# Kernel tuning notes

Hardware: AMD Instinct MI355X
Metric: run time of the kernel (lower is better)

## Reference

```python
import jax, jax.numpy as jnp
import numpy as np

H = 1024      # hidden_size
NH = 16       # num attention heads
NKV = 4       # num kv heads (GQA)
HD = 64       # head_dim
NE = 8        # num experts
TOPK = 2      # experts per token
F = 2048      # expert intermediate size
T = 2048      # num tokens
EPS = 1e-5
THETA = 10000.0


def rmsnorm(x, w):
    var = jnp.mean(x * x, axis=-1, keepdims=True)
    return x * jax.lax.rsqrt(var + EPS) * w


def apply_rope(x, positions):
    # x: [T, nheads, HD], neox style (rotate halves)
    half = HD // 2
    inv_freq = 1.0 / (THETA ** (jnp.arange(half, dtype=jnp.float32) / half))
    ang = positions.astype(jnp.float32)[:, None] * inv_freq  # [T, half]
    cos = jnp.cos(ang)[:, None, :]
    sin = jnp.sin(ang)[:, None, :]
    x1, x2 = x[..., :half], x[..., half:]
    return jnp.concatenate([x1 * cos - x2 * sin, x2 * cos + x1 * sin], axis=-1)


def attention(x, positions, w_qkv, w_o):
    qkv = x @ w_qkv.T                                  # [T, (NH+2*NKV)*HD]
    q = qkv[:, : NH * HD].reshape(T, NH, HD)
    k = qkv[:, NH * HD : (NH + NKV) * HD].reshape(T, NKV, HD)
    v = qkv[:, (NH + NKV) * HD :].reshape(T, NKV, HD)
    q = apply_rope(q, positions)
    k = apply_rope(k, positions)
    rep = NH // NKV
    k = jnp.repeat(k, rep, axis=1)                     # [T, NH, HD]
    v = jnp.repeat(v, rep, axis=1)
    scores = jnp.einsum('qhd,khd->hqk', q, k) * (HD ** -0.5)
    mask = jnp.tril(jnp.ones((T, T), dtype=bool))
    scores = jnp.where(mask[None], scores, jnp.finfo(scores.dtype).min)
    p = jax.nn.softmax(scores, axis=-1)
    o = jnp.einsum('hqk,khd->qhd', p, v).reshape(T, NH * HD)
    return o @ w_o.T


def moe(x, gate_w, w1, w2, w3):
    logits = x @ gate_w.T                              # [T, NE]
    probs = jax.nn.softmax(logits, axis=-1)
    tv, ti = jax.lax.top_k(probs, TOPK)
    tv = tv / jnp.sum(tv, axis=-1, keepdims=True)      # renormalize=True
    dense = jnp.zeros((x.shape[0], NE), x.dtype).at[
        jnp.arange(x.shape[0])[:, None], ti].set(tv)   # [T, NE] sparse routing weights
    h1 = jnp.einsum('th,efh->tef', x, w1)
    h3 = jnp.einsum('th,efh->tef', x, w3)
    act = jax.nn.silu(h1) * h3                         # SwiGLU
    y = jnp.einsum('tef,ehf->teh', act, w2)
    return jnp.einsum('te,teh->th', dense, y)


def setup_inputs() -> dict:
    key = jax.random.key(0)
    ks = jax.random.split(key, 8)
    s = 0.02
    return {
        'positions': jnp.arange(T, dtype=jnp.int32),
        'hidden_states': jax.random.normal(ks[0], (T, H), jnp.float32),
        'w_qkv': jax.random.normal(ks[1], ((NH + 2 * NKV) * HD, H), jnp.float32) * s,
        'w_o': jax.random.normal(ks[2], (H, NH * HD), jnp.float32) * s,
        'norm_in': jnp.ones((H,), jnp.float32),
        'norm_post': jnp.ones((H,), jnp.float32),
        'norm_next': jnp.ones((H,), jnp.float32),
        'gate_w': jax.random.normal(ks[3], (NE, H), jnp.float32) * s,
        'w1': jax.random.normal(ks[4], (NE, F, H), jnp.float32) * s,
        'w2': jax.random.normal(ks[5], (NE, H, F), jnp.float32) * s,
        'w3': jax.random.normal(ks[6], (NE, F, H), jnp.float32) * s,
    }


def reference(positions, hidden_states, w_qkv, w_o, norm_in, norm_post, norm_next,
              gate_w, w1, w2, w3):
    # attn block: pre-norm, attention, residual add
    x = hidden_states + attention(rmsnorm(hidden_states, norm_in), positions, w_qkv, w_o)
    # moe block: pre-norm, sparse MoE, residual add
    x = x + moe(rmsnorm(x, norm_post), gate_w, w1, w2, w3)
    # fused allreduce+norm boundary -> next layer's input norm (world_size=1)
    out = rmsnorm(x, norm_next)
    return (out, x)
```

## Files before the change

### kernel.cpp

```cpp
#include <hip/hip_runtime.h>
#include <hip/hip_bf16.h>
#include <stdint.h>

#define T 2048
#define H 1024
#define NH 16
#define NKV 4
#define HD 64
#define NE 8
#define FF 2048
#define QKVD 1536

typedef unsigned short u16;
typedef short bf16x8 __attribute__((ext_vector_type(8)));
typedef float f32x4 __attribute__((ext_vector_type(4)));

__device__ __forceinline__ float bf2f(u16 u) { return __uint_as_float(((unsigned)u) << 16); }
__device__ __forceinline__ u16 f2b(float f) {
    unsigned u = __float_as_uint(f);
    unsigned r = (u + 0x7FFFu + ((u >> 16) & 1u)) >> 16;
    return (u16)r;
}

#define MFMA(a, b, c) __builtin_amdgcn_mfma_f32_16x16x32_bf16(a, b, c, 0, 0, 0)

__device__ __forceinline__ void gll16(const u16* g, u16* l) {
    __builtin_amdgcn_global_load_lds(
        (const __attribute__((address_space(1))) void*)g,
        (__attribute__((address_space(3))) void*)l, 16, 0, 0);
}

__global__ __launch_bounds__(256) void k_cvt(const float* __restrict__ src,
                                             u16* __restrict__ dst) {
    size_t i = ((size_t)blockIdx.x * 256 + threadIdx.x) * 8;
    float4 a = *(const float4*)(src + i);
    float4 b = *(const float4*)(src + i + 4);
    bf16x8 o;
    o[0] = (short)f2b(a.x); o[1] = (short)f2b(a.y);
    o[2] = (short)f2b(a.z); o[3] = (short)f2b(a.w);
    o[4] = (short)f2b(b.x); o[5] = (short)f2b(b.y);
    o[6] = (short)f2b(b.z); o[7] = (short)f2b(b.w);
    *(bf16x8*)(dst + i) = o;
}

__global__ __launch_bounds__(256) void k_rmsnorm(const float* __restrict__ x,
                                                 const float* __restrict__ w,
                                                 u16* __restrict__ out) {
    int t = blockIdx.x;
    const float* xr = x + (size_t)t * H;
    int base = threadIdx.x * 4;
    float v[4]; float ss = 0.f;
#pragma unroll
    for (int i = 0; i < 4; i++) { v[i] = xr[base + i]; ss += v[i] * v[i]; }
#pragma unroll
    for (int off = 32; off; off >>= 1) ss += __shfl_xor(ss, off, 64);
    __shared__ float red[4];
    int wv = threadIdx.x >> 6, lane = threadIdx.x & 63;
    if (lane == 0) red[wv] = ss;
    __syncthreads();
    float tot = red[0] + red[1] + red[2] + red[3];
    float s = rsqrtf(tot * (1.0f / H) + 1e-5f);
    u16* orow = out + (size_t)t * H;
#pragma unroll
    for (int i = 0; i < 4; i++) orow[base + i] = f2b(v[i] * s * w[base + i]);
}

__global__ __launch_bounds__(256) void k_gemm_qkv(const u16* __restrict__ A,
                                                  const u16* __restrict__ B,
                                                  float* __restrict__ C) {
    __shared__ u16 As[128 * 32], Bs[128 * 32];
    const int K = H;
    int lane = threadIdx.x & 63, wv = threadIdx.x >> 6;
    int l15 = lane & 15, quad = lane >> 4;
    int gm = blockIdx.y * 128, gn = blockIdx.x * 128;
    int c0 = wv * 128 + lane, c1 = c0 + 64;
    int r0 = c0 >> 2, cc0 = (c0 & 3) * 8;
    int r1 = c1 >> 2, cc1 = (c1 & 3) * 8;
    const u16* ag0 = A + (size_t)(gm + r0) * K + cc0;
    const u16* ag1 = A + (size_t)(gm + r1) * K + cc1;
    const u16* bg0 = B + (size_t)(gn + r0) * K + cc0;
    const u16* bg1 = B + (size_t)(gn + r1) * K + cc1;
    u16* la0 = As + (size_t)(wv * 128) * 8;
    u16* la1 = As + (size_t)(wv * 128 + 64) * 8;
    u16* lb0 = Bs + (size_t)(wv * 128) * 8;
    u16* lb1 = Bs + (size_t)(wv * 128 + 64) * 8;
    int am = (wv >> 1) * 64, bn = (wv & 1) * 64;
    f32x4 acc[4][4];
#pragma unroll
    for (int i = 0; i < 4; i++)
#pragma unroll
        for (int j = 0; j < 4; j++) acc[i][j] = (f32x4){0.f, 0.f, 0.f, 0.f};
    for (int kk = 0; kk < K; kk += 32) {
        gll16(ag0 + kk, la0);
        gll16(ag1 + kk, la1);
        gll16(bg0 + kk, lb0);
        gll16(bg1 + kk, lb1);
        __syncthreads();
        bf16x8 a[4], b[4];
#pragma unroll
        for (int i = 0; i < 4; i++) a[i] = *(const bf16x8*)(As + (am + i * 16 + l15) * 32 + quad * 8);
#pragma unroll
        for (int j = 0; j < 4; j++) b[j] = *(const bf16x8*)(Bs + (bn + j * 16 + l15) * 32 + quad * 8);
#pragma unroll
        for (int i = 0; i < 4; i++)
#pragma unroll
            for (int j = 0; j < 4; j++) acc[i][j] = MFMA(a[i], b[j], acc[i][j]);
        __syncthreads();
    }
#pragma unroll
    for (int i = 0; i < 4; i++) {
        int row = gm + am + i * 16 + quad * 4;
#pragma unroll
        for (int j = 0; j < 4; j++) {
            int col = gn + bn + j * 16 + l15;
#pragma unroll
            for (int r = 0; r < 4; r++) C[(size_t)(row + r) * QKVD + col] = acc[i][j][r];
        }
    }
}

__global__ __launch_bounds__(256) void k_rope(const int* __restrict__ positions,
                                              const float* __restrict__ qkv,
                                              u16* __restrict__ qb, u16* __restrict__ kb,
                                              u16* __restrict__ vt) {
    int t = blockIdx.x;
    float p = (float)positions[t];
    const float* base = qkv + (size_t)t * QKVD;
    const float kfreq = -9.210340371976184f / 32.0f;
    for (int idx = threadIdx.x; idx < 512; idx += 256) {
        int hh = idx >> 5, d = idx & 31;
        float ang = p * __expf((float)d * kfreq);
        float cs = cosf(ang), sn = sinf(ang);
        float x1 = base[hh * 64 + d], x2 = base[hh * 64 + d + 32];
        qb[(size_t)t * 1024 + hh * 64 + d] = f2b(x1 * cs - x2 * sn);
        qb[(size_t)t * 1024 + hh * 64 + d + 32] = f2b(x2 * cs + x1 * sn);
    }
    if (threadIdx.x < 128) {
        int idx = threadIdx.x, kh = idx >> 5, d = idx & 31;
        float ang = p * __expf((float)d * kfreq);
        float cs = cosf(ang), sn = sinf(ang);
        const float* kin = base + 1024;
        float x1 = kin[kh * 64 + d], x2 = kin[kh * 64 + d + 32];
        kb[((size_t)t * NKV + kh) * 64 + d] = f2b(x1 * cs - x2 * sn);
        kb[((size_t)t * NKV + kh) * 64 + d + 32] = f2b(x2 * cs + x1 * sn);
    }
    {
        int idx = threadIdx.x;
        vt[(size_t)idx * T + t] = f2b(base[1280 + idx]);
    }
}

__global__ __launch_bounds__(256) void k_attn(const u16* __restrict__ qb,
                                              const u16* __restrict__ kb,
                                              const u16* __restrict__ vt,
                                              u16* __restrict__ o) {
    int h = blockIdx.y;
    int q0 = blockIdx.x * 64;
    int kh = h >> 2;
    int wv = threadIdx.x >> 6, lane = threadIdx.x & 63;
    int l15 = lane & 15, quad = lane >> 4;
    int qw = q0 + wv * 16;
    __shared__ __align__(16) u16 pl[4][16 * 32];

    const u16* qrow = qb + (size_t)(qw + l15) * 1024 + h * 64 + quad * 8;
    bf16x8 aq0 = *(const bf16x8*)qrow;
    bf16x8 aq1 = *(const bf16x8*)(qrow + 32);

    f32x4 oacc[4];
#pragma unroll
    for (int c = 0; c < 4; c++) oacc[c] = (f32x4){0.f, 0.f, 0.f, 0.f};
    float mi[4], li[4];
#pragma unroll
    for (int r = 0; r < 4; r++) { mi[r] = -3e38f; li[r] = 0.f; }

    int ntiles = (q0 >> 5) + 2;
    for (int ti = 0; ti < ntiles; ++ti) {
        int kv0 = ti * 32;
        const u16* kr = kb + (size_t)((kv0 + l15) * NKV + kh) * 64 + quad * 8;
        f32x4 sA = (f32x4){0.f, 0.f, 0.f, 0.f}, sB = (f32x4){0.f, 0.f, 0.f, 0.f};
        sA = MFMA(aq0, *(const bf16x8*)kr, sA);
        sA = MFMA(aq1, *(const bf16x8*)(kr + 32), sA);
        const u16* kr2 = kr + 16 * NKV * 64;
        sB = MFMA(aq0, *(const bf16x8*)kr2, sB);
        sB = MFMA(aq1, *(const bf16x8*)(kr2 + 32), sB);
        int cA = kv0 + l15, cB = cA + 16;
#pragma unroll
        for (int r = 0; r < 4; r++) {
            int qi = qw + quad * 4 + r;
            float a = (cA <= qi) ? sA[r] * 0.125f : -3e38f;
            float b = (cB <= qi) ? sB[r] * 0.125f : -3e38f;
            float mx = fmaxf(a, b);
#pragma unroll
            for (int off = 1; off < 16; off <<= 1) mx = fmaxf(mx, __shfl_xor(mx, off, 64));
            float mn = fmaxf(mi[r], mx);
            float alpha = __expf(mi[r] - mn);
            float pa = __expf(a - mn), pb = __expf(b - mn);
            float ps = pa + pb;
#pragma unroll
            for (int off = 1; off < 16; off <<= 1) ps += __shfl_xor(ps, off, 64);
            li[r] = li[r] * alpha + ps;
            mi[r] = mn;
#pragma unroll
            for (int c = 0; c < 4; c++) oacc[c][r] = oacc[c][r] * alpha;
            int prow = quad * 4 + r;
            pl[wv][prow * 32 + l15] = f2b(pa);
            pl[wv][prow * 32 + 16 + l15] = f2b(pb);
        }
        __syncthreads();
        bf16x8 pfrag = *(const bf16x8*)&pl[wv][l15 * 32 + quad * 8];
#pragma unroll
        for (int c = 0; c < 4; c++) {
            const u16* vr = vt + (size_t)(kh * 64 + c * 16 + l15) * T + kv0 + quad * 8;
            oacc[c] = MFMA(pfrag, *(const bf16x8*)vr, oacc[c]);
        }
        __syncthreads();
    }
#pragma unroll
    for (int r = 0; r < 4; r++) {
        float inv = 1.0f / li[r];
        int row = qw + quad * 4 + r;
#pragma unroll
        for (int c = 0; c < 4; c++)
            o[(size_t)row * 1024 + h * 64 + c * 16 + l15] = f2b(oacc[c][r] * inv);
    }
}

__global__ __launch_bounds__(256) void k_gemm_wo(const u16* __restrict__ A,
                                                 const u16* __restrict__ B,
                                                 const float* __restrict__ hid,
                                                 float* __restrict__ x1) {
    __shared__ u16 As[128 * 32], Bs[128 * 32];
    const int K = H;
    int lane = threadIdx.x & 63, wv = threadIdx.x >> 6;
    int l15 = lane & 15, quad = lane >> 4;
    int gm = blockIdx.y * 128, gn = blockIdx.x * 128;
    int c0 = wv * 128 + lane, c1 = c0 + 64;
    int r0 = c0 >> 2, cc0 = (c0 & 3) * 8;
    int r1 = c1 >> 2, cc1 = (c1 & 3) * 8;
    const u16* ag0 = A + (size_t)(gm + r0) * K + cc0;
    const u16* ag1 = A + (size_t)(gm + r1) * K + cc1;
    const u16* bg0 = B + (size_t)(gn + r0) * K + cc0;
    const u16* bg1 = B + (size_t)(gn + r1) * K + cc1;
    u16* la0 = As + (size_t)(wv * 128) * 8;
    u16* la1 = As + (size_t)(wv * 128 + 64) * 8;
    u16* lb0 = Bs + (size_t)(wv * 128) * 8;
    u16* lb1 = Bs + (size_t)(wv * 128 + 64) * 8;
    int am = (wv >> 1) * 64, bn = (wv & 1) * 64;
    f32x4 acc[4][4];
#pragma unroll
    for (int i = 0; i < 4; i++)
#pragma unroll
        for (int j = 0; j < 4; j++) acc[i][j] = (f32x4){0.f, 0.f, 0.f, 0.f};
    for (int kk = 0; kk < K; kk += 32) {
        gll16(ag0 + kk, la0);
        gll16(ag1 + kk, la1);
        gll16(bg0 + kk, lb0);
        gll16(bg1 + kk, lb1);
        __syncthreads();
        bf16x8 a[4], b[4];
#pragma unroll
        for (int i = 0; i < 4; i++) a[i] = *(const bf16x8*)(As + (am + i * 16 + l15) * 32 + quad * 8);
#pragma unroll
        for (int j = 0; j < 4; j++) b[j] = *(const bf16x8*)(Bs + (bn + j * 16 + l15) * 32 + quad * 8);
#pragma unroll
        for (int i = 0; i < 4; i++)
#pragma unroll
            for (int j = 0; j < 4; j++) acc[i][j] = MFMA(a[i], b[j], acc[i][j]);
        __syncthreads();
    }
#pragma unroll
    for (int i = 0; i < 4; i++) {
        int row = gm + am + i * 16 + quad * 4;
#pragma unroll
        for (int j = 0; j < 4; j++) {
            int col = gn + bn + j * 16 + l15;
#pragma unroll
            for (int r = 0; r < 4; r++) {
                size_t idx = (size_t)(row + r) * H + col;
                x1[idx] = hid[idx] + acc[i][j][r];
            }
        }
    }
}

__global__ void k_zero(int* cnt) { if (threadIdx.x < NE) cnt[threadIdx.x] = 0; }

__global__ __launch_bounds__(256) void k_route(const float* __restrict__ x1,
                                               const float* __restrict__ wpost,
                                               const float* __restrict__ gw,
                                               int* cnt, int* ids, int* rank,
                                               float* gwt) {
    int wv = threadIdx.x >> 6, lane = threadIdx.x & 63;
    int t = blockIdx.x * 4 + wv;
    const float* xr = x1 + (size_t)t * H + lane * 16;
    float pv[16];
    float ss = 0.f;
#pragma unroll
    for (int i = 0; i < 16; i++) { float v = xr[i]; pv[i] = v; ss += v * v; }
#pragma unroll
    for (int off = 32; off; off >>= 1) ss += __shfl_xor(ss, off, 64);
    float s = rsqrtf(ss * (1.0f / H) + 1e-5f);
#pragma unroll
    for (int i = 0; i < 16; i++) pv[i] *= wpost[lane * 16 + i];
    float lg[NE];
#pragma unroll
    for (int e = 0; e < NE; e++) {
        const float* gr = gw + (size_t)e * H + lane * 16;
        float d = 0.f;
#pragma unroll
        for (int i = 0; i < 16; i++) d += pv[i] * gr[i];
#pragma unroll
        for (int off = 32; off; off >>= 1) d += __shfl_xor(d, off, 64);
        lg[e] = d * s;
    }
    if (lane == 0) {
        int i0 = 0; float b0 = lg[0];
        for (int e = 1; e < NE; e++) if (lg[e] > b0) { b0 = lg[e]; i0 = e; }
        int i1 = (i0 == 0) ? 1 : 0; float b1 = lg[i1];
        for (int e = 0; e < NE; e++)
            if (e != i0 && lg[e] > b1) { b1 = lg[e]; i1 = e; }
        float g0 = 1.0f / (1.0f + __expf(b1 - b0));
        float g1 = 1.0f - g0;
        int r0 = atomicAdd(&cnt[i0], 1);
        int r1 = atomicAdd(&cnt[i1], 1);
        ids[2 * t] = i0; ids[2 * t + 1] = i1;
        rank[2 * t] = r0; rank[2 * t + 1] = r1;
        gwt[2 * t] = g0; gwt[2 * t + 1] = g1;
    }
}

__global__ void k_prefix(const int* cnt, int* offs) {
    if (threadIdx.x == 0) {
        int a = 0;
        for (int e = 0; e < NE; e++) { offs[e] = a; a += cnt[e]; }
    }
}

__global__ __launch_bounds__(256) void k_scatter(const int* __restrict__ ids,
                                                 const int* __restrict__ rank,
                                                 const int* __restrict__ offs,
                                                 int* __restrict__ list,
                                                 int* __restrict__ slotof) {
    int t = blockIdx.x * 256 + threadIdx.x;
#pragma unroll
    for (int j = 0; j < 2; j++) {
        int e = ids[2 * t + j];
        int s = offs[e] + rank[2 * t + j];
        list[s] = t;
        slotof[2 * t + j] = s;
    }
}

__global__ __launch_bounds__(256, 2) void k_gemm1(const u16* __restrict__ xnp,
                                                  const u16* __restrict__ w1,
                                                  const u16* __restrict__ w3,
                                                  const int* __restrict__ cnt,
                                                  const int* __restrict__ offs,
                                                  const int* __restrict__ list,
                                                  u16* __restrict__ act) {
    int e = blockIdx.z;
    int ce = cnt[e], oe = offs[e];
    int gm = blockIdx.y * 128;
    if (gm >= ce) return;
    __shared__ u16 As[128 * 32], B1s[128 * 32], B3s[128 * 32];
    const int K = H;
    int lane = threadIdx.x & 63, wv = threadIdx.x >> 6;
    int l15 = lane & 15, quad = lane >> 4;
    int gn = blockIdx.x * 128;
    int c0 = wv * 128 + lane, c1 = c0 + 64;
    int r0 = c0 >> 2, cc0 = (c0 & 3) * 8;
    int r1 = c1 >> 2, cc1 = (c1 & 3) * 8;
    int tok0 = list[min(oe + gm + r0, oe + ce - 1)];
    int tok1 = list[min(oe + gm + r1, oe + ce - 1)];
    const u16* ag0 = xnp + (size_t)tok0 * K + cc0;
    const u16* ag1 = xnp + (size_t)tok1 * K + cc1;
    const u16* B1 = w1 + (size_t)e * FF * H;
    const u16* B3 = w3 + (size_t)e * FF * H;
    const u16* b1g0 = B1 + (size_t)(gn + r0) * K + cc0;
    const u16* b1g1 = B1 + (size_t)(gn + r1) * K + cc1;
    const u16* b3g0 = B3 + (size_t)(gn + r0) * K + cc0;
    const u16* b3g1 = B3 + (size_t)(gn + r1) * K + cc1;
    u16* la0 = As + (size_t)(wv * 128) * 8;
    u16* la1 = As + (size_t)(wv * 128 + 64) * 8;
    u16* l10 = B1s + (size_t)(wv * 128) * 8;
    u16* l11 = B1s + (size_t)(wv * 128 + 64) * 8;
    u16* l30 = B3s + (size_t)(wv * 128) * 8;
    u16* l31 = B3s + (size_t)(wv * 128 + 64) * 8;
    int am = (wv >> 1) * 64, bn = (wv & 1) * 64;
    f32x4 a1[4][4], a3[4][4];
#pragma unroll
    for (int i = 0; i < 4; i++)
#pragma unroll
        for (int j = 0; j < 4; j++) {
            a1[i][j] = (f32x4){0.f, 0.f, 0.f, 0.f};
            a3[i][j] = (f32x4){0.f, 0.f, 0.f, 0.f};
        }
    for (int kk = 0; kk < K; kk += 32) {
        gll16(ag0 + kk, la0);
        gll16(ag1 + kk, la1);
        gll16(b1g0 + kk, l10);
        gll16(b1g1 + kk, l11);
        gll16(b3g0 + kk, l30);
        gll16(b3g1 + kk, l31);
        __syncthreads();
        bf16x8 a[4], b1v[4], b3v[4];
#pragma unroll
        for (int i = 0; i < 4; i++) a[i] = *(const bf16x8*)(As + (am + i * 16 + l15) * 32 + quad * 8);
#pragma unroll
        for (int j = 0; j < 4; j++) {
            b1v[j] = *(const bf16x8*)(B1s + (bn + j * 16 + l15) * 32 + quad * 8);
            b3v[j] = *(const bf16x8*)(B3s + (bn + j * 16 + l15) * 32 + quad * 8);
        }
#pragma unroll
        for (int i = 0; i < 4; i++)
#pragma unroll
            for (int j = 0; j < 4; j++) {
                a1[i][j] = MFMA(a[i], b1v[j], a1[i][j]);
                a3[i][j] = MFMA(a[i], b3v[j], a3[i][j]);
            }
        __syncthreads();
    }
#pragma unroll
    for (int i = 0; i < 4; i++) {
        int rb = gm + am + i * 16 + quad * 4;
#pragma unroll
        for (int r = 0; r < 4; r++) {
            int row = rb + r;
            if (row < ce) {
#pragma unroll
                for (int j = 0; j < 4; j++) {
                    int col = gn + bn + j * 16 + l15;
                    float h1 = a1[i][j][r], h3 = a3[i][j][r];
                    float sv = h1 / (1.0f + __expf(-h1));
                    act[(size_t)(oe + row) * FF + col] = f2b(sv * h3);
                }
            }
        }
    }
}

__global__ __launch_bounds__(256) void k_gemm2(const u16* __restrict__ act,
                                               const u16* __restrict__ w2,
                                               const int* __restrict__ cnt,
                                               const int* __restrict__ offs,
                                               float* __restrict__ y) {
    int e = blockIdx.z;
    int ce = cnt[e], oe = offs[e];
    int gm = blockIdx.y * 128;
    if (gm >= ce) return;
    __shared__ u16 As[128 * 32], Bs[128 * 32];
    const int K = FF;
    int lane = threadIdx.x & 63, wv = threadIdx.x >> 6;
    int l15 = lane & 15, quad = lane >> 4;
    int gn = blockIdx.x * 128;
    int c0 = wv * 128 + lane, c1 = c0 + 64;
    int r0 = c0 >> 2, cc0 = (c0 & 3) * 8;
    int r1 = c1 >> 2, cc1 = (c1 & 3) * 8;
    int sr0 = min(oe + gm + r0, oe + ce - 1);
    int sr1 = min(oe + gm + r1, oe + ce - 1);
    const u16* ag0 = act + (size_t)sr0 * K + cc0;
    const u16* ag1 = act + (size_t)sr1 * K + cc1;
    const u16* B = w2 + (size_t)e * H * FF;
    const u16* bg0 = B + (size_t)(gn + r0) * K + cc0;
    const u16* bg1 = B + (size_t)(gn + r1) * K + cc1;
    u16* la0 = As + (size_t)(wv * 128) * 8;
    u16* la1 = As + (size_t)(wv * 128 + 64) * 8;
    u16* lb0 = Bs + (size_t)(wv * 128) * 8;
    u16* lb1 = Bs + (size_t)(wv * 128 + 64) * 8;
    int am = (wv >> 1) * 64, bn = (wv & 1) * 64;
    f32x4 acc[4][4];
#pragma unroll
    for (int i = 0; i < 4; i++)
#pragma unroll
        for (int j = 0; j < 4; j++) acc[i][j] = (f32x4){0.f, 0.f, 0.f, 0.f};
    for (int kk = 0; kk < K; kk += 32) {
        gll16(ag0 + kk, la0);
        gll16(ag1 + kk, la1);
        gll16(bg0 + kk, lb0);
        gll16(bg1 + kk, lb1);
        __syncthreads();
        bf16x8 a[4], b[4];
#pragma unroll
        for (int i = 0; i < 4; i++) a[i] = *(const bf16x8*)(As + (am + i * 16 + l15) * 32 + quad * 8);
#pragma unroll
        for (int j = 0; j < 4; j++) b[j] = *(const bf16x8*)(Bs + (bn + j * 16 + l15) * 32 + quad * 8);
#pragma unroll
        for (int i = 0; i < 4; i++)
#pragma unroll
            for (int j = 0; j < 4; j++) acc[i][j] = MFMA(a[i], b[j], acc[i][j]);
        __syncthreads();
    }
#pragma unroll
    for (int i = 0; i < 4; i++) {
        int rb = gm + am + i * 16 + quad * 4;
#pragma unroll
        for (int r = 0; r < 4; r++) {
            int row = rb + r;
            if (row < ce) {
#pragma unroll
                for (int j = 0; j < 4; j++) {
                    int col = gn + bn + j * 16 + l15;
                    y[(size_t)(oe + row) * H + col] = acc[i][j][r];
                }
            }
        }
    }
}

__global__ __launch_bounds__(256) void k_combine(const float* __restrict__ x1,
                                                 const float* __restrict__ y,
                                                 const int* __restrict__ slotof,
                                                 const float* __restrict__ gwt,
                                                 const float* __restrict__ wnext,
                                                 float* __restrict__ dout) {
    int t = blockIdx.x;
    int s0 = slotof[2 * t], s1 = slotof[2 * t + 1];
    float g0 = gwt[2 * t], g1 = gwt[2 * t + 1];
    int base = threadIdx.x * 4;
    float v[4]; float ss = 0.f;
#pragma unroll
    for (int i = 0; i < 4; i++) {
        int idx = base + i;
        float val = x1[(size_t)t * H + idx] + g0 * y[(size_t)s0 * H + idx] + g1 * y[(size_t)s1 * H + idx];
        v[i] = val; ss += val * val;
    }
#pragma unroll
    for (int off = 32; off; off >>= 1) ss += __shfl_xor(ss, off, 64);
    __shared__ float red[4];
    int wv = threadIdx.x >> 6, lane = threadIdx.x & 63;
    if (lane == 0) red[wv] = ss;
    __syncthreads();
    float tot = red[0] + red[1] + red[2] + red[3];
    float s = rsqrtf(tot * (1.0f / H) + 1e-5f);
#pragma unroll
    for (int i = 0; i < 4; i++) {
        int idx = base + i;
        dout[(size_t)t * H + idx] = v[i] * s * wnext[idx];
        dout[(size_t)T * H + (size_t)t * H + idx] = v[i];
    }
}

extern "C" void kernel_launch(void* const* d_in, const int* in_sizes, int n_in,
                              void* d_out, int out_size, void* d_ws, size_t ws_size,
                              hipStream_t stream) {
    (void)in_sizes; (void)n_in; (void)out_size; (void)ws_size;
    const int*   positions = (const int*)d_in[0];
    const float* hidden    = (const float*)d_in[1];
    const float* w_qkv     = (const float*)d_in[2];
    const float* w_o       = (const float*)d_in[3];
    const float* norm_in   = (const float*)d_in[4];
    const float* norm_post = (const float*)d_in[5];
    const float* norm_next = (const float*)d_in[6];
    const float* gate_w    = (const float*)d_in[7];
    const float* w1        = (const float*)d_in[8];
    const float* w2        = (const float*)d_in[9];
    const float* w3        = (const float*)d_in[10];

    char* ws = (char*)d_ws;
    const size_t MB = (size_t)1 << 20;
    u16*   wqb  = (u16*)(ws + 0 * MB);
    u16*   wob  = (u16*)(ws + 3 * MB);
    u16*   w1b  = (u16*)(ws + 5 * MB);
    u16*   w2b  = (u16*)(ws + 37 * MB);
    u16*   w3b  = (u16*)(ws + 69 * MB);
    u16*   xn_in= (u16*)(ws + 101 * MB);
    float* qkv  = (float*)(ws + 105 * MB);
    u16*   qb   = (u16*)(ws + 117 * MB);
    u16*   kbuf = (u16*)(ws + 121 * MB);
    u16*   vt   = (u16*)(ws + 122 * MB);
    u16*   obuf = (u16*)(ws + 123 * MB);
    float* x1   = (float*)(ws + 127 * MB);
    u16*   xnp  = (u16*)(ws + 101 * MB);
    u16*   act  = (u16*)(ws + 105 * MB);
    float* yb   = (float*)(ws + 135 * MB);
    char*  rt   = ws + 151 * MB;
    int*   cnt    = (int*)(rt);
    int*   offs   = (int*)(rt + 64);
    int*   ids    = (int*)(rt + 128);
    int*   rank   = (int*)(rt + 128 + 16384);
    float* gwt    = (float*)(rt + 128 + 2 * 16384);
    int*   slotof = (int*)(rt + 128 + 3 * 16384);
    int*   list   = (int*)(rt + 128 + 4 * 16384);
    float* dout   = (float*)d_out;

    k_cvt<<<dim3(QKVD * H / 2048), dim3(256), 0, stream>>>(w_qkv, wqb);
    k_cvt<<<dim3(H * H / 2048), dim3(256), 0, stream>>>(w_o, wob);
    k_cvt<<<dim3(NE * FF * H / 2048), dim3(256), 0, stream>>>(w1, w1b);
    k_cvt<<<dim3(NE * H * FF / 2048), dim3(256), 0, stream>>>(w2, w2b);
    k_cvt<<<dim3(NE * FF * H / 2048), dim3(256), 0, stream>>>(w3, w3b);

    k_rmsnorm<<<dim3(T), dim3(256), 0, stream>>>(hidden, norm_in, xn_in);
    k_gemm_qkv<<<dim3(QKVD / 128, T / 128), dim3(256), 0, stream>>>(xn_in, wqb, qkv);
    k_rope<<<dim3(T), dim3(256), 0, stream>>>(positions, qkv, qb, kbuf, vt);
    k_attn<<<dim3(T / 64, NH), dim3(256), 0, stream>>>(qb, kbuf, vt, obuf);
    k_gemm_wo<<<dim3(H / 128, T / 128), dim3(256), 0, stream>>>(obuf, wob, hidden, x1);
    k_rmsnorm<<<dim3(T), dim3(256), 0, stream>>>(x1, norm_post, xnp);
    k_zero<<<dim3(1), dim3(64), 0, stream>>>(cnt);
    k_route<<<dim3(T / 4), dim3(256), 0, stream>>>(x1, norm_post, gate_w, cnt, ids, rank, gwt);
    k_prefix<<<dim3(1), dim3(1), 0, stream>>>(cnt, offs);
    k_scatter<<<dim3(T / 256), dim3(256), 0, stream>>>(ids, rank, offs, list, slotof);
    k_gemm1<<<dim3(FF / 128, T / 128, NE), dim3(256), 0, stream>>>(xnp, w1b, w3b, cnt, offs, list, act);
    k_gemm2<<<dim3(H / 128, T / 128, NE), dim3(256), 0, stream>>>(act, w2b, cnt, offs, yb);
    k_combine<<<dim3(T), dim3(256), 0, stream>>>(x1, yb, slotof, gwt, norm_next, dout);
}
```

Baseline: 633.1 us.

## Widen attention KV tiles to 64, drop barriers, balance causal work, merge expert weight casts

The attention kernel now handles 64 keys per step instead of 32, which halves the number of online-softmax passes and shuffle reductions per key. It drops the two __syncthreads per tile, since each wave only reads its own LDS slice. The grid becomes 1D and orders blocks so light and heavy causal q-tiles are interleaved, aiming for better load balance. The three expert weight conversions are merged into one launch to cut launch overhead, and a 64-wide last tile still relies on masking to handle the diagonal correctly.

After: 597.3 us. 5.7% less time.

```diff
diff --git a/kernel.cpp b/kernel.cpp
--- a/kernel.cpp
+++ b/kernel.cpp
@@ -30,8 +30,8 @@
         (__attribute__((address_space(3))) void*)l, 16, 0, 0);
 }
 
-__global__ __launch_bounds__(256) void k_cvt(const float* __restrict__ src,
-                                             u16* __restrict__ dst) {
+__device__ __forceinline__ void cvt_body(const float* __restrict__ src,
+                                         u16* __restrict__ dst) {
     size_t i = ((size_t)blockIdx.x * 256 + threadIdx.x) * 8;
     float4 a = *(const float4*)(src + i);
     float4 b = *(const float4*)(src + i + 4);
@@ -41,6 +41,21 @@
     o[4] = (short)f2b(b.x); o[5] = (short)f2b(b.y);
     o[6] = (short)f2b(b.z); o[7] = (short)f2b(b.w);
     *(bf16x8*)(dst + i) = o;
+}
+
+__global__ __launch_bounds__(256) void k_cvt(const float* __restrict__ src,
+                                             u16* __restrict__ dst) {
+    cvt_body(src, dst);
+}
+
+__global__ __launch_bounds__(256) void k_cvt3(const float* __restrict__ s0, u16* __restrict__ d0,
+                                              const float* __restrict__ s1, u16* __restrict__ d1,
+                                              const float* __restrict__ s2, u16* __restrict__ d2) {
+    const float* s; u16* d;
+    if (blockIdx.y == 0) { s = s0; d = d0; }
+    else if (blockIdx.y == 1) { s = s1; d = d1; }
+    else { s = s2; d = d2; }
+    cvt_body(s, d);
 }
 
 __global__ __launch_bounds__(256) void k_rmsnorm(const float* __restrict__ x,
@@ -154,66 +169,80 @@
                                               const u16* __restrict__ kb,
                                               const u16* __restrict__ vt,
                                               u16* __restrict__ o) {
-    int h = blockIdx.y;
-    int q0 = blockIdx.x * 64;
+    int g = blockIdx.x;
+    int pair = g & 255, sel = g >> 8;
+    int h = pair & 15, qt = pair >> 4;
+    int qtile = sel ? (31 - qt) : qt;
+    int q0 = qtile * 64;
     int kh = h >> 2;
     int wv = threadIdx.x >> 6, lane = threadIdx.x & 63;
     int l15 = lane & 15, quad = lane >> 4;
     int qw = q0 + wv * 16;
-    __shared__ __align__(16) u16 pl[4][16 * 32];
+    __shared__ __align__(16) u16 pl[4][16 * 64];
+    u16* plw = pl[wv];
+    const f32x4 zero4 = {0.f, 0.f, 0.f, 0.f};
 
     const u16* qrow = qb + (size_t)(qw + l15) * 1024 + h * 64 + quad * 8;
     bf16x8 aq0 = *(const bf16x8*)qrow;
     bf16x8 aq1 = *(const bf16x8*)(qrow + 32);
 
+    const u16* kbase = kb + kh * 64 + quad * 8;
+    const u16* vbase = vt + (size_t)(kh * 64) * T + quad * 8;
+
     f32x4 oacc[4];
 #pragma unroll
-    for (int c = 0; c < 4; c++) oacc[c] = (f32x4){0.f, 0.f, 0.f, 0.f};
+    for (int c = 0; c < 4; c++) oacc[c] = zero4;
     float mi[4], li[4];
 #pragma unroll
     for (int r = 0; r < 4; r++) { mi[r] = -3e38f; li[r] = 0.f; }
 
-    int ntiles = (q0 >> 5) + 2;
+    int ntiles = qtile + 1;
     for (int ti = 0; ti < ntiles; ++ti) {
-        int kv0 = ti * 32;
-        const u16* kr = kb + (size_t)((kv0 + l15) * NKV + kh) * 64 + quad * 8;
-        f32x4 sA = (f32x4){0.f, 0.f, 0.f, 0.f}, sB = (f32x4){0.f, 0.f, 0.f, 0.f};
-        sA = MFMA(aq0, *(const bf16x8*)kr, sA);
-        sA = MFMA(aq1, *(const bf16x8*)(kr + 32), sA);
-        const u16* kr2 = kr + 16 * NKV * 64;
-        sB = MFMA(aq0, *(const bf16x8*)kr2, sB);
-        sB = MFMA(aq1, *(const bf16x8*)(kr2 + 32), sB);
-        int cA = kv0 + l15, cB = cA + 16;
+        int kv0 = ti * 64;
+        f32x4 sC[4];
+#pragma unroll
+        for (int c = 0; c < 4; c++) {
+            const u16* kr = kbase + (size_t)(kv0 + c * 16 + l15) * (NKV * 64);
+            sC[c] = MFMA(aq0, *(const bf16x8*)kr, zero4);
+            sC[c] = MFMA(aq1, *(const bf16x8*)(kr + 32), sC[c]);
+        }
 #pragma unroll
         for (int r = 0; r < 4; r++) {
             int qi = qw + quad * 4 + r;
-            float a = (cA <= qi) ? sA[r] * 0.125f : -3e38f;
-            float b = (cB <= qi) ? sB[r] * 0.125f : -3e38f;
-            float mx = fmaxf(a, b);
+            float sc[4];
+#pragma unroll
+            for (int c = 0; c < 4; c++) {
+                int col = kv0 + c * 16 + l15;
+                sc[c] = (col <= qi) ? sC[c][r] * 0.125f : -3e38f;
+            }
+            float mx = fmaxf(fmaxf(sc[0], sc[1]), fmaxf(sc[2], sc[3]));
 #pragma unroll
             for (int off = 1; off < 16; off <<= 1) mx = fmaxf(mx, __shfl_xor(mx, off, 64));
             float mn = fmaxf(mi[r], mx);
             float alpha = __expf(mi[r] - mn);
-            float pa = __expf(a - mn), pb = __expf(b - mn);
-            float ps = pa + pb;
+            float p0 = __expf(sc[0] - mn), p1 = __expf(sc[1] - mn);
+            float p2 = __expf(sc[2] - mn), p3 = __expf(sc[3] - mn);
+            float ps = (p0 + p1) + (p2 + p3);
 #pragma unroll
             for (int off = 1; off < 16; off <<= 1) ps += __shfl_xor(ps, off, 64);
             li[r] = li[r] * alpha + ps;
             mi[r] = mn;
 #pragma unroll
-            for (int c = 0; c < 4; c++) oacc[c][r] = oacc[c][r] * alpha;
+            for (int c = 0; c < 4; c++) oacc[c][r] *= alpha;
             int prow = quad * 4 + r;
-            pl[wv][prow * 32 + l15] = f2b(pa);
-            pl[wv][prow * 32 + 16 + l15] = f2b(pb);
-        }
-        __syncthreads();
-        bf16x8 pfrag = *(const bf16x8*)&pl[wv][l15 * 32 + quad * 8];
+            plw[prow * 64 + l15] = f2b(p0);
+            plw[prow * 64 + 16 + l15] = f2b(p1);
+            plw[prow * 64 + 32 + l15] = f2b(p2);
+            plw[prow * 64 + 48 + l15] = f2b(p3);
+        }
+        bf16x8 pf0 = *(const bf16x8*)&plw[l15 * 64 + quad * 8];
+        bf16x8 pf1 = *(const bf16x8*)&plw[l15 * 64 + 32 + quad * 8];
 #pragma unroll
         for (int c = 0; c < 4; c++) {
-            const u16* vr = vt + (size_t)(kh * 64 + c * 16 + l15) * T + kv0 + quad * 8;
-            oacc[c] = MFMA(pfrag, *(const bf16x8*)vr, oacc[c]);
-        }
-        __syncthreads();
+            const u16* vr = vbase + (size_t)(c * 16 + l15) * T + kv0;
+            oacc[c] = MFMA(pf0, *(const bf16x8*)vr, oacc[c]);
+            oacc[c] = MFMA(pf1, *(const bf16x8*)(vr + 32), oacc[c]);
+        }
     }
 #pragma unroll
     for (int r = 0; r < 4; r++) {
@@ -585,14 +614,12 @@
 
     k_cvt<<<dim3(QKVD * H / 2048), dim3(256), 0, stream>>>(w_qkv, wqb);
     k_cvt<<<dim3(H * H / 2048), dim3(256), 0, stream>>>(w_o, wob);
-    k_cvt<<<dim3(NE * FF * H / 2048), dim3(256), 0, stream>>>(w1, w1b);
-    k_cvt<<<dim3(NE * H * FF / 2048), dim3(256), 0, stream>>>(w2, w2b);
-    k_cvt<<<dim3(NE * FF * H / 2048), dim3(256), 0, stream>>>(w3, w3b);
+    k_cvt3<<<dim3(NE * FF * H / 2048, 3), dim3(256), 0, stream>>>(w1, w1b, w2, w2b, w3, w3b);
 
     k_rmsnorm<<<dim3(T), dim3(256), 0, stream>>>(hidden, norm_in, xn_in);
     k_gemm_qkv<<<dim3(QKVD / 128, T / 128), dim3(256), 0, stream>>>(xn_in, wqb, qkv);
     k_rope<<<dim3(T), dim3(256), 0, stream>>>(positions, qkv, qb, kbuf, vt);
-    k_attn<<<dim3(T / 64, NH), dim3(256), 0, stream>>>(qb, kbuf, vt, obuf);
+    k_attn<<<dim3(512), dim3(256), 0, stream>>>(qb, kbuf, vt, obuf);
     k_gemm_wo<<<dim3(H / 128, T / 128), dim3(256), 0, stream>>>(obuf, wob, hidden, x1);
     k_rmsnorm<<<dim3(T), dim3(256), 0, stream>>>(x1, norm_post, xnp);
     k_zero<<<dim3(1), dim3(64), 0, stream>>>(cnt);
```
